# Kernel optimization log

Hardware: AMD Instinct MI355X
Metric: run time of the kernel (lower is better)

## Reference

```python
import jax, jax.numpy as jnp
import numpy as np

ALPHA = 0.1

def setup_inputs() -> dict:
    key = jax.random.key(0)
    k1, k2, k3, k4 = jax.random.split(key, 4)
    B, T, D_IN, H, R = 32, 2048, 128, 512, 2
    x = jax.random.normal(k1, (B, T, D_IN), dtype=jnp.float32)
    m = jax.random.normal(k2, (H, R), dtype=jnp.float32) / np.sqrt(H)
    n = jax.random.normal(k3, (H, R), dtype=jnp.float32) / np.sqrt(H)
    I = jax.random.normal(k4, (H, D_IN), dtype=jnp.float32) / np.sqrt(H)
    return {"x": x, "m": m, "n": n, "I": I}

def reference(x, m, n, I):
    # x: [B, T, D_in]; m,n: [H, R]; I: [H, D_in]
    B = x.shape[0]
    H = m.shape[0]
    J = m @ n.T  # [H, H] low-rank recurrent matrix, as in the torch module
    # Precompute input projection for all timesteps: (I @ x_t^T)^T == x_t @ I^T
    x_proj = jnp.einsum('btd,hd->bth', x, I)  # [B, T, H]
    h0 = jnp.zeros((B, H), dtype=x.dtype)

    def step(h, xp_t):
        dh = -h + jnp.tanh(h) @ J.T + xp_t  # (J @ tanh(h)^T)^T == tanh(h) @ J^T
        h = h + ALPHA * dh
        return h, h

    _, hiddens = jax.lax.scan(step, h0, jnp.swapaxes(x_proj, 0, 1))  # [T, B, H]
    return jnp.swapaxes(hiddens, 0, 1)  # [B, T, H]
```

## Files before the change

### kernel.cpp

```cpp
#include <hip/hip_runtime.h>


#define ALPHA 0.1f
typedef float v2 __attribute__((ext_vector_type(2)));
typedef short s16x8 __attribute__((ext_vector_type(8)));
typedef float f32x4 __attribute__((ext_vector_type(4)));
typedef unsigned short u16x8 __attribute__((ext_vector_type(8)));
typedef __attribute__((address_space(1))) ushort g_u16;
typedef __attribute__((address_space(3))) ushort l_u16;

__device__ __forceinline__ ushort f2bf(float x) {
  uint u = __float_as_uint(x);
  return (ushort)((u + 0x7FFFu + ((u >> 16) & 1u)) >> 16);
}
__device__ __forceinline__ int swz(int row, int k) {
  return row * 128 + (k ^ ((row & 7) << 3));
}

#define MFMA __builtin_amdgcn_mfma_f32_16x16x32_bf16

__global__ __launch_bounds__(256)
void to_bf16_swz(const float* __restrict__ X, const float* __restrict__ Iw,
                 ushort* __restrict__ Xh, ushort* __restrict__ Ih) {
  const int b = blockIdx.x;
  const float* src;
  ushort* dh;
  int gid;
  if (b < 4096) {
    src = X; dh = Xh; gid = b * 256 + threadIdx.x;
  } else {
    src = Iw; dh = Ih; gid = (b - 4096) * 256 + threadIdx.x;
  }
  const int row = gid >> 4;
  const int k0 = (gid & 15) * 8;
  const float4* p = (const float4*)(src + (size_t)row * 128 + k0);
  float4 a = p[0], bq = p[1];
  float v[8] = {a.x, a.y, a.z, a.w, bq.x, bq.y, bq.z, bq.w};
  u16x8 hi;
#pragma unroll
  for (int i = 0; i < 8; ++i) hi[i] = f2bf(v[i]);
  const int ks = k0 ^ ((row & 7) << 3);
  *(u16x8*)&dh[(size_t)row * 128 + ks] = hi;
}

__global__ __launch_bounds__(256, 4)
void xproj_gemm2(const ushort* __restrict__ Xh, const ushort* __restrict__ Ih,
                 float* __restrict__ C) {
  __shared__ ushort Ahs[64 * 128];
  __shared__ ushort Bhs[64 * 128];

  const int u = blockIdx.x;
  const int m0 = ((u & 7) * 128 + (u >> 6)) * 64;
  const int n0 = ((u >> 3) & 7) * 64;

  const int id = threadIdx.x;
  const int lane = id & 63;
  const int wid = id >> 6;

  {
    const int half = (wid & 1) * 32;
    const ushort* g;
    ushort* l;
    if (wid < 2) { g = Xh + (size_t)(m0 + half) * 128; l = Ahs + half * 128; }
    else         { g = Ih + (size_t)(n0 + half) * 128; l = Bhs + half * 128; }
    g += lane * 8;
#pragma unroll
    for (int i = 0; i < 8; ++i)
      __builtin_amdgcn_global_load_lds((const g_u16*)(g + i * 512),
                                       (l_u16*)(l + i * 512), 16, 0, 0);
  }
  __syncthreads();

  const int wr = (wid >> 1) * 32;
  const int wc = (wid & 1) * 32;
  const int fr = lane & 15;
  const int fk = (lane >> 4) * 8;

  f32x4 acc[2][2] = {};

#pragma unroll
  for (int kk = 0; kk < 4; ++kk) {
    const int kb = kk * 32 + fk;
    s16x8 ahi[2], bhi[2];
#pragma unroll
    for (int i = 0; i < 2; ++i)
      ahi[i] = *(const s16x8*)&Ahs[swz(wr + i * 16 + fr, kb)];
#pragma unroll
    for (int jn = 0; jn < 2; ++jn)
      bhi[jn] = *(const s16x8*)&Bhs[swz(wc + jn * 16 + fr, kb)];
#pragma unroll
    for (int i = 0; i < 2; ++i)
#pragma unroll
      for (int jn = 0; jn < 2; ++jn)
        acc[i][jn] = MFMA(ahi[i], bhi[jn], acc[i][jn], 0, 0, 0);
  }

#pragma unroll
  for (int i = 0; i < 2; ++i)
#pragma unroll
    for (int jn = 0; jn < 2; ++jn) {
      int r0 = m0 + wr + i * 16 + (lane >> 4) * 4;
      int c0 = n0 + wc + jn * 16 + (lane & 15);
#pragma unroll
      for (int t = 0; t < 4; ++t)
        C[(size_t)(r0 + t) * 512 + c0] = acc[i][jn][t];
    }
}

__global__ __launch_bounds__(256, 2)
void xproj_gemm_fused(const float* __restrict__ X, const float* __restrict__ Iw,
                      float* __restrict__ C) {
  __shared__ ushort Ahs[64 * 128];
  __shared__ ushort Bhs[64 * 128];

  const int u = blockIdx.x;
  const int m0 = ((u & 7) * 128 + (u >> 6)) * 64;
  const int n0 = ((u >> 3) & 7) * 64;
  const int id = threadIdx.x;

#pragma unroll
  for (int j = 0; j < 8; ++j) {
    int f = id + 256 * j;
    int row = f >> 5, c4 = f & 31;
    int k0 = 4 * c4;
    float4 a4 = *(const float4*)(X + (size_t)(m0 + row) * 128 + k0);
    float4 b4 = *(const float4*)(Iw + (size_t)(n0 + row) * 128 + k0);
    int sa = swz(row, k0);
    *(ushort4*)&Ahs[sa] =
        make_ushort4(f2bf(a4.x), f2bf(a4.y), f2bf(a4.z), f2bf(a4.w));
    *(ushort4*)&Bhs[sa] =
        make_ushort4(f2bf(b4.x), f2bf(b4.y), f2bf(b4.z), f2bf(b4.w));
  }
  __syncthreads();

  const int lane = id & 63;
  const int wid = id >> 6;
  const int wr = (wid >> 1) * 32;
  const int wc = (wid & 1) * 32;
  const int fr = lane & 15;
  const int fk = (lane >> 4) * 8;

  f32x4 acc[2][2] = {};
#pragma unroll
  for (int kk = 0; kk < 4; ++kk) {
    const int kb = kk * 32 + fk;
    s16x8 ahi[2], bhi[2];
#pragma unroll
    for (int i = 0; i < 2; ++i)
      ahi[i] = *(const s16x8*)&Ahs[swz(wr + i * 16 + fr, kb)];
#pragma unroll
    for (int jn = 0; jn < 2; ++jn)
      bhi[jn] = *(const s16x8*)&Bhs[swz(wc + jn * 16 + fr, kb)];
#pragma unroll
    for (int i = 0; i < 2; ++i)
#pragma unroll
      for (int jn = 0; jn < 2; ++jn)
        acc[i][jn] = MFMA(ahi[i], bhi[jn], acc[i][jn], 0, 0, 0);
  }
#pragma unroll
  for (int i = 0; i < 2; ++i)
#pragma unroll
    for (int jn = 0; jn < 2; ++jn) {
      int r0 = m0 + wr + i * 16 + (lane >> 4) * 4;
      int c0 = n0 + wc + jn * 16 + (lane & 15);
#pragma unroll
      for (int t = 0; t < 4; ++t)
        C[(size_t)(r0 + t) * 512 + c0] = acc[i][jn][t];
    }
}

#define DPP_STEP(v, ctrl)                                                     \
  ((v) + __int_as_float(__builtin_amdgcn_update_dpp(                          \
             0, __float_as_int(v), (ctrl), 0xf, 0xf, true)))

__device__ __forceinline__ float wave_sum63(float v) {
  v = DPP_STEP(v, 0x111);
  v = DPP_STEP(v, 0x112);
  v = DPP_STEP(v, 0x114);
  v = DPP_STEP(v, 0x118);
  v = DPP_STEP(v, 0x142);
  v = DPP_STEP(v, 0x143);
  return v;
}

struct ScanState {
  v2 m0v[4], m1v[4], n0v[4], n1v[4], hv[4];
};

__device__ __forceinline__ void scan_init(ScanState& S, const float* mw,
                                          const float* nw, int base) {
  const float2* mp = (const float2*)mw;
  const float2* np = (const float2*)nw;
#pragma unroll
  for (int p = 0; p < 4; ++p) {
    float2 ma = mp[base + 2 * p], mb = mp[base + 2 * p + 1];
    float2 na = np[base + 2 * p], nb = np[base + 2 * p + 1];
    S.m0v[p] = (v2){ma.x, mb.x};
    S.m1v[p] = (v2){ma.y, mb.y};
    S.n0v[p] = (v2){ALPHA * na.x, ALPHA * nb.x};
    S.n1v[p] = (v2){ALPHA * na.y, ALPHA * nb.y};
    S.hv[p] = (v2){0.f, 0.f};
  }
}

__device__ __forceinline__ void scan_step(ScanState& S, float4 xa, float4 xb) {
  const v2 TC0 = (v2){-5.70498872745e-3f, -5.70498872745e-3f};
  const v2 TC1 = (v2){2.06390887954e-2f, 2.06390887954e-2f};
  const v2 TC2 = (v2){-5.37397155531e-2f, -5.37397155531e-2f};
  const v2 TC3 = (v2){1.33314422036e-1f, 1.33314422036e-1f};
  const v2 TC4 = (v2){-3.33332819422e-1f, -3.33332819422e-1f};
  const v2 CLO = (v2){-1.15f, -1.15f};
  const v2 CHI = (v2){1.15f, 1.15f};
  const v2 K9 = (v2){1.f - ALPHA, 1.f - ALPHA};
  const v2 KA = (v2){ALPHA, ALPHA};

  v2 xpv[4] = {(v2){xa.x, xa.y}, (v2){xa.z, xa.w},
               (v2){xb.x, xb.y}, (v2){xb.z, xb.w}};
  v2 p0 = (v2){0.f, 0.f}, p1 = (v2){0.f, 0.f};
#pragma unroll
  for (int p = 0; p < 4; ++p) {
    v2 xc = __builtin_elementwise_min(
        __builtin_elementwise_max(S.hv[p], CLO), CHI);
    v2 z = xc * xc;
    v2 q = __builtin_elementwise_fma(z, TC0, TC1);
    q = __builtin_elementwise_fma(z, q, TC2);
    q = __builtin_elementwise_fma(z, q, TC3);
    q = __builtin_elementwise_fma(z, q, TC4);
    v2 th = __builtin_elementwise_fma(xc * z, q, xc);
    p0 = __builtin_elementwise_fma(th, S.n0v[p], p0);
    p1 = __builtin_elementwise_fma(th, S.n1v[p], p1);
  }
  float s0 = wave_sum63(p0.x + p0.y);
  float s1 = wave_sum63(p1.x + p1.y);
  s0 = __int_as_float(__builtin_amdgcn_readlane(__float_as_int(s0), 63));
  s1 = __int_as_float(__builtin_amdgcn_readlane(__float_as_int(s1), 63));
  v2 s0v = (v2){s0, s0}, s1v = (v2){s1, s1};
#pragma unroll
  for (int p = 0; p < 4; ++p) {
    v2 d = __builtin_elementwise_fma(s0v, S.m0v[p], s1v * S.m1v[p]);
    S.hv[p] = __builtin_elementwise_fma(
        K9, S.hv[p], __builtin_elementwise_fma(KA, xpv[p], d));
  }
}

#define CS 64
#define CW 96

__global__ __launch_bounds__(64, 1)
void rnn_scan_chunk(const float* __restrict__ mw, const float* __restrict__ nw,
                    const float* __restrict__ xp, float* __restrict__ out) {
  const int b = blockIdx.x;
  const int c = blockIdx.y;
  const int base = threadIdx.x * 8;

  ScanState S;
  scan_init(S, mw, nw, base);

  const float* xrow = xp + (size_t)b * 2048 * 512 + base;
  float* orow = out + (size_t)b * 2048 * 512 + base;

  const int t1 = c * CS;
  int t0 = t1 - CW;
  if (t0 < 0) t0 = 0;
  const int t2 = t1 + CS;
  const int warm_blocks = (t1 - t0) >> 3;
  const int tot_blocks = (t2 - t0) >> 3;

  float4 ra[8], rb[8];
#pragma unroll
  for (int u = 0; u < 8; ++u) {
    ra[u] = *(const float4*)(xrow + (size_t)(t0 + u) * 512);
    rb[u] = *(const float4*)(xrow + (size_t)(t0 + u) * 512 + 4);
  }

  for (int bb = 0; bb < tot_blocks; ++bb) {
    const int tb = t0 + bb * 8;
    const bool refill = (bb + 1 < tot_blocks);
    const bool dostore = (bb >= warm_blocks);
#pragma unroll
    for (int u = 0; u < 8; ++u) {
      float4 xa = ra[u], xb = rb[u];
      if (refill) {
        ra[u] = *(const float4*)(xrow + (size_t)(tb + 8 + u) * 512);
        rb[u] = *(const float4*)(xrow + (size_t)(tb + 8 + u) * 512 + 4);
      }
      scan_step(S, xa, xb);
      if (dostore) {
        *(float4*)(orow + (size_t)(tb + u) * 512) =
            make_float4(S.hv[0].x, S.hv[0].y, S.hv[1].x, S.hv[1].y);
        *(float4*)(orow + (size_t)(tb + u) * 512 + 4) =
            make_float4(S.hv[2].x, S.hv[2].y, S.hv[3].x, S.hv[3].y);
      }
    }
  }
}

__global__ __launch_bounds__(64, 1)
void rnn_scan_serial(const float* __restrict__ mw, const float* __restrict__ nw,
                     float* __restrict__ out) {
  const int b = blockIdx.x;
  const int base = threadIdx.x * 8;
  ScanState S;
  scan_init(S, mw, nw, base);
  float* row = out + (size_t)b * 2048 * 512 + base;

  float4 ra[8], rb[8];
#pragma unroll
  for (int u = 0; u < 8; ++u) {
    ra[u] = *(const float4*)(row + (size_t)u * 512);
    rb[u] = *(const float4*)(row + (size_t)u * 512 + 4);
  }
  for (int bb = 0; bb < 256; ++bb) {
    const int tb = bb * 8;
    const bool refill = (bb + 1 < 256);
#pragma unroll
    for (int u = 0; u < 8; ++u) {
      float4 xa = ra[u], xb = rb[u];
      if (refill) {
        ra[u] = *(const float4*)(row + (size_t)(tb + 8 + u) * 512);
        rb[u] = *(const float4*)(row + (size_t)(tb + 8 + u) * 512 + 4);
      }
      scan_step(S, xa, xb);
      *(float4*)(row + (size_t)(tb + u) * 512) =
          make_float4(S.hv[0].x, S.hv[0].y, S.hv[1].x, S.hv[1].y);
      *(float4*)(row + (size_t)(tb + u) * 512 + 4) =
          make_float4(S.hv[2].x, S.hv[2].y, S.hv[3].x, S.hv[3].y);
    }
  }
}

extern "C" void kernel_launch(void* const* d_in, const int* in_sizes, int n_in,
                              void* d_out, int out_size, void* d_ws, size_t ws_size,
                              hipStream_t stream) {
  const float* x  = (const float*)d_in[0];
  const float* mw = (const float*)d_in[1];
  const float* nw = (const float*)d_in[2];
  const float* Iw = (const float*)d_in[3];
  float* out = (float*)d_out;

  const size_t xp_bytes = 32ull * 2048ull * 512ull * 4ull;

  if (ws_size >= xp_bytes) {
    float* xp = (float*)d_ws;
    ushort* Xh = (ushort*)out;
    ushort* Ih = Xh + 65536ull * 128ull;
    to_bf16_swz<<<4128, 256, 0, stream>>>(x, Iw, Xh, Ih);
    xproj_gemm2<<<8192, 256, 0, stream>>>(Xh, Ih, xp);
    rnn_scan_chunk<<<dim3(32, 32), 64, 0, stream>>>(mw, nw, xp, out);
  } else {
    xproj_gemm_fused<<<8192, 256, 0, stream>>>(x, Iw, out);
    rnn_scan_serial<<<32, 64, 0, stream>>>(mw, nw, out);
  }
}
```

Before: 250.1 us.

## Store input projection as bf16 and use smaller scan chunks with nontemporal stores

The GEMM now writes the x projection as bf16 instead of fp32, halving the workspace traffic, and the chunked scan reads bf16 and widens to fp32. The scan chunk size drops from 64 to 32 timesteps, doubling the grid to 2048 blocks for more parallelism at the cost of more redundant warm-up steps per chunk. Output stores become nontemporal. Rounding the projection to bf16 adds error to the recurrence input.

```diff
diff --git a/kernel.cpp b/kernel.cpp
--- a/kernel.cpp
+++ b/kernel.cpp
@@ -12,6 +12,9 @@
 __device__ __forceinline__ ushort f2bf(float x) {
   uint u = __float_as_uint(x);
   return (ushort)((u + 0x7FFFu + ((u >> 16) & 1u)) >> 16);
+}
+__device__ __forceinline__ float bf2f(ushort h) {
+  return __uint_as_float(((uint)h) << 16);
 }
 __device__ __forceinline__ int swz(int row, int k) {
   return row * 128 + (k ^ ((row & 7) << 3));
@@ -45,7 +48,7 @@
 
 __global__ __launch_bounds__(256, 4)
 void xproj_gemm2(const ushort* __restrict__ Xh, const ushort* __restrict__ Ih,
-                 float* __restrict__ C) {
+                 ushort* __restrict__ C) {
   __shared__ ushort Ahs[64 * 128];
   __shared__ ushort Bhs[64 * 128];
 
@@ -103,7 +106,7 @@
       int c0 = n0 + wc + jn * 16 + (lane & 15);
 #pragma unroll
       for (int t = 0; t < 4; ++t)
-        C[(size_t)(r0 + t) * 512 + c0] = acc[i][jn][t];
+        C[(size_t)(r0 + t) * 512 + c0] = f2bf(acc[i][jn][t]);
     }
 }
 
@@ -203,7 +206,7 @@
   }
 }
 
-__device__ __forceinline__ void scan_step(ScanState& S, float4 xa, float4 xb) {
+__device__ __forceinline__ void scan_step(ScanState& S, u16x8 xr) {
   const v2 TC0 = (v2){-5.70498872745e-3f, -5.70498872745e-3f};
   const v2 TC1 = (v2){2.06390887954e-2f, 2.06390887954e-2f};
   const v2 TC2 = (v2){-5.37397155531e-2f, -5.37397155531e-2f};
@@ -214,8 +217,11 @@
   const v2 K9 = (v2){1.f - ALPHA, 1.f - ALPHA};
   const v2 KA = (v2){ALPHA, ALPHA};
 
-  v2 xpv[4] = {(v2){xa.x, xa.y}, (v2){xa.z, xa.w},
-               (v2){xb.x, xb.y}, (v2){xb.z, xb.w}};
+  v2 xpv[4];
+#pragma unroll
+  for (int p = 0; p < 4; ++p)
+    xpv[p] = (v2){bf2f(xr[2 * p]), bf2f(xr[2 * p + 1])};
+
   v2 p0 = (v2){0.f, 0.f}, p1 = (v2){0.f, 0.f};
 #pragma unroll
   for (int p = 0; p < 4; ++p) {
@@ -243,12 +249,12 @@
   }
 }
 
-#define CS 64
+#define CS 32
 #define CW 96
 
 __global__ __launch_bounds__(64, 1)
 void rnn_scan_chunk(const float* __restrict__ mw, const float* __restrict__ nw,
-                    const float* __restrict__ xp, float* __restrict__ out) {
+                    const ushort* __restrict__ xp, float* __restrict__ out) {
   const int b = blockIdx.x;
   const int c = blockIdx.y;
   const int base = threadIdx.x * 8;
@@ -256,7 +262,7 @@
   ScanState S;
   scan_init(S, mw, nw, base);
 
-  const float* xrow = xp + (size_t)b * 2048 * 512 + base;
+  const ushort* xrow = xp + (size_t)b * 2048 * 512 + base;
   float* orow = out + (size_t)b * 2048 * 512 + base;
 
   const int t1 = c * CS;
@@ -266,12 +272,10 @@
   const int warm_blocks = (t1 - t0) >> 3;
   const int tot_blocks = (t2 - t0) >> 3;
 
-  float4 ra[8], rb[8];
-#pragma unroll
-  for (int u = 0; u < 8; ++u) {
-    ra[u] = *(const float4*)(xrow + (size_t)(t0 + u) * 512);
-    rb[u] = *(const float4*)(xrow + (size_t)(t0 + u) * 512 + 4);
-  }
+  u16x8 ra[8];
+#pragma unroll
+  for (int u = 0; u < 8; ++u)
+    ra[u] = *(const u16x8*)(xrow + (size_t)(t0 + u) * 512);
 
   for (int bb = 0; bb < tot_blocks; ++bb) {
     const int tb = t0 + bb * 8;
@@ -279,19 +283,58 @@
     const bool dostore = (bb >= warm_blocks);
 #pragma unroll
     for (int u = 0; u < 8; ++u) {
-      float4 xa = ra[u], xb = rb[u];
-      if (refill) {
-        ra[u] = *(const float4*)(xrow + (size_t)(tb + 8 + u) * 512);
-        rb[u] = *(const float4*)(xrow + (size_t)(tb + 8 + u) * 512 + 4);
-      }
-      scan_step(S, xa, xb);
+      u16x8 xr = ra[u];
+      if (refill)
+        ra[u] = *(const u16x8*)(xrow + (size_t)(tb + 8 + u) * 512);
+      scan_step(S, xr);
       if (dostore) {
-        *(float4*)(orow + (size_t)(tb + u) * 512) =
-            make_float4(S.hv[0].x, S.hv[0].y, S.hv[1].x, S.hv[1].y);
-        *(float4*)(orow + (size_t)(tb + u) * 512 + 4) =
-            make_float4(S.hv[2].x, S.hv[2].y, S.hv[3].x, S.hv[3].y);
+        f32x4 o0 = {S.hv[0].x, S.hv[0].y, S.hv[1].x, S.hv[1].y};
+        f32x4 o1 = {S.hv[2].x, S.hv[2].y, S.hv[3].x, S.hv[3].y};
+        __builtin_nontemporal_store(o0, (f32x4*)(orow + (size_t)(tb + u) * 512));
+        __builtin_nontemporal_store(o1, (f32x4*)(orow + (size_t)(tb + u) * 512 + 4));
       }
     }
+  }
+}
+
+__device__ __forceinline__ void scan_step_f32(ScanState& S, float4 xa, float4 xb) {
+  u16x8 dummy;
+  const v2 TC0 = (v2){-5.70498872745e-3f, -5.70498872745e-3f};
+  const v2 TC1 = (v2){2.06390887954e-2f, 2.06390887954e-2f};
+  const v2 TC2 = (v2){-5.37397155531e-2f, -5.37397155531e-2f};
+  const v2 TC3 = (v2){1.33314422036e-1f, 1.33314422036e-1f};
+  const v2 TC4 = (v2){-3.33332819422e-1f, -3.33332819422e-1f};
+  const v2 CLO = (v2){-1.15f, -1.15f};
+  const v2 CHI = (v2){1.15f, 1.15f};
+  const v2 K9 = (v2){1.f - ALPHA, 1.f - ALPHA};
+  const v2 KA = (v2){ALPHA, ALPHA};
+  (void)dummy;
+  v2 xpv[4] = {(v2){xa.x, xa.y}, (v2){xa.z, xa.w},
+               (v2){xb.x, xb.y}, (v2){xb.z, xb.w}};
+  v2 p0 = (v2){0.f, 0.f}, p1 = (v2){0.f, 0.f};
+#pragma unroll
+  for (int p = 0; p < 4; ++p) {
+    v2 xc = __builtin_elementwise_min(
+        __builtin_elementwise_max(S.hv[p], CLO), CHI);
+    v2 z = xc * xc;
+    v2 q = __builtin_elementwise_fma(z, TC0, TC1);
+    q = __builtin_elementwise_fma(z, q, TC2);
+    q = __builtin_elementwise_fma(z, q, TC3);
+    q = __builtin_elementwise_fma(z, q, TC4);
+    v2 th = __builtin_elementwise_fma(xc * z, q, xc);
+    p0 = __builtin_elementwise_fma(th, S.n0v[p], p0);
+    p1 = __builtin_elementwise_fma(th, S.n1v[p], p1);
+  }
+  float s0 = wave_sum63(p0.x + p0.y);
+  float s1 = wave_sum63(p1.x + p1.y);
+  s0 = __int_as_float(__builtin_amdgcn_readlane(__float_as_int(s0), 63));
+  s1 = __int_as_float(__builtin_amdgcn_readlane(__float_as_int(s1), 63));
+  v2 s0v = (v2){s0, s0}, s1v = (v2){s1, s1};
+#pragma unroll
+  for (int p = 0; p < 4; ++p) {
+    v2 d = __builtin_elementwise_fma(s0v, S.m0v[p], s1v * S.m1v[p]);
+    S.hv[p] = __builtin_elementwise_fma(
+        K9, S.hv[p], __builtin_elementwise_fma(KA, xpv[p], d));
   }
 }
 
@@ -320,7 +363,7 @@
         ra[u] = *(const float4*)(row + (size_t)(tb + 8 + u) * 512);
         rb[u] = *(const float4*)(row + (size_t)(tb + 8 + u) * 512 + 4);
       }
-      scan_step(S, xa, xb);
+      scan_step_f32(S, xa, xb);
       *(float4*)(row + (size_t)(tb + u) * 512) =
           make_float4(S.hv[0].x, S.hv[0].y, S.hv[1].x, S.hv[1].y);
       *(float4*)(row + (size_t)(tb + u) * 512 + 4) =
@@ -338,15 +381,15 @@
   const float* Iw = (const float*)d_in[3];
   float* out = (float*)d_out;
 
-  const size_t xp_bytes = 32ull * 2048ull * 512ull * 4ull;
+  const size_t xp_bytes = 32ull * 2048ull * 512ull * 2ull;
 
   if (ws_size >= xp_bytes) {
-    float* xp = (float*)d_ws;
+    ushort* xp = (ushort*)d_ws;
     ushort* Xh = (ushort*)out;
     ushort* Ih = Xh + 65536ull * 128ull;
     to_bf16_swz<<<4128, 256, 0, stream>>>(x, Iw, Xh, Ih);
     xproj_gemm2<<<8192, 256, 0, stream>>>(Xh, Ih, xp);
-    rnn_scan_chunk<<<dim3(32, 32), 64, 0, stream>>>(mw, nw, xp, out);
+    rnn_scan_chunk<<<dim3(32, 2048 / CS), 64, 0, stream>>>(mw, nw, xp, out);
   } else {
     xproj_gemm_fused<<<8192, 256, 0, stream>>>(x, Iw, out);
     rnn_scan_serial<<<32, 64, 0, stream>>>(mw, nw, out);
```

Result: faster. 242.3 us (-3.1%).
